# Performance work log

Measured on AMD Instinct MI355X. Metric: run time of the kernel, lower is better.

The kernel has to match this reference:

```python
import jax, jax.numpy as jnp
import numpy as np

EPS = 1e-8
TOP_K = 2


def _l2norm(v, axis=-1):
    # F.normalize: v / max(||v||_2, eps)
    n = jnp.sqrt(jnp.sum(v * v, axis=axis, keepdims=True))
    return v / jnp.maximum(n, EPS)


def setup_inputs() -> dict:
    key = jax.random.key(0)
    ks = jax.random.split(key, 5)
    B, S, D, F, E = 2, 2048, 512, 2048, 8
    x = jax.random.normal(ks[0], (B, S, D), dtype=jnp.float32)
    anchors = jax.random.normal(ks[1], (E, D), dtype=jnp.float32)
    W1 = jax.random.normal(ks[2], (E, D, F), dtype=jnp.float32) * (1.0 / np.sqrt(D))
    b1 = jnp.zeros((E, F), dtype=jnp.float32)
    W2 = jax.random.normal(ks[3], (E, F, D), dtype=jnp.float32) * (1.0 / np.sqrt(F))
    b2 = jnp.zeros((E, D), dtype=jnp.float32)
    return {"x": x, "anchors": anchors, "W1": W1, "b1": b1, "W2": W2, "b2": b2}


def reference(x, anchors, W1, b1, W2, b2):
    B, S, D = x.shape
    E = anchors.shape[0]
    x_flat = x.reshape(B * S, D)  # (T, D)

    # Semantic resonance routing: cosine similarity with anchors
    x_n = _l2norm(x_flat)
    a_n = _l2norm(anchors)
    scores = jnp.einsum('td,ed->te', x_n, a_n)  # (T, E)

    # Noisy top-k (eval mode: no noise) + softmax gates over top-k scores
    topk_scores, topk_idx = jax.lax.top_k(scores, TOP_K)  # (T, K)
    gates = jax.nn.softmax(topk_scores, axis=-1)  # (T, K)

    # Combine weights per (token, expert); top-k indices are distinct per token
    T = B * S
    combine = jnp.zeros((T, E), dtype=x.dtype)
    combine = combine.at[jnp.arange(T)[:, None], topk_idx].add(gates)

    # Per-expert MLP (Linear -> exact GELU -> Linear), combined by gates.
    # Dense-over-experts form is mathematically identical to the sorted
    # grouped dispatch + index_add in the original module.
    h = jnp.einsum('td,edf->tef', x_flat, W1) + b1[None]  # (T, E, F)
    h = jax.nn.gelu(h, approximate=False)
    y = jnp.einsum('tef,efd->ted', h, W2) + b2[None]  # (T, E, D)
    out_flat = jnp.einsum('te,ted->td', combine, y)  # (T, D)

    out = out_flat.reshape(B, S, D)
    # aux_data equivalents: anchors_norm, resonance_scores, topk_indices
    return out, a_n, scores, topk_idx
```

## Files before the change

kernel.cpp:

```cpp
#include <hip/hip_runtime.h>
#include <cstdint>


#define T_TOK 4096
#define D_DIM 512
#define F_DIM 2048
#define E_EXP 8
#define NROWS 9216
#define MAXTILES 72

typedef __bf16 bf16x8 __attribute__((ext_vector_type(8)));
typedef float  f32x4  __attribute__((ext_vector_type(4)));
typedef unsigned short u16;

__device__ __forceinline__ u16 f2b(float f) {
    return __builtin_bit_cast(unsigned short, (__bf16)f);
}
__device__ __forceinline__ void gload16(void* lds, const void* g) {
    __builtin_amdgcn_global_load_lds(
        (const __attribute__((address_space(1))) void*)g,
        (__attribute__((address_space(3))) void*)lds, 16, 0, 0);
}
__device__ __forceinline__ float gelu_f(float v) {
    float z = 0.7978845608f * (v + 0.044715f * v * v * v);
    float t = 1.0f - 2.0f / (1.0f + __expf(2.0f * z));
    return 0.5f * v * (1.0f + t);
}

__global__ void init_k(int* __restrict__ cnt, int* __restrict__ rowmap,
                       float* __restrict__ rowgate, float* __restrict__ outm) {
    int tid = blockIdx.x * 256 + threadIdx.x;
    int nth = gridDim.x * 256;
    if (tid < E_EXP) cnt[tid] = 0;
    for (int i = tid; i < NROWS; i += nth) { rowmap[i] = -1; rowgate[i] = 0.f; }
    float4* o4 = (float4*)outm;
    for (int i = tid; i < (T_TOK * D_DIM) / 4; i += nth)
        o4[i] = float4{0.f, 0.f, 0.f, 0.f};
}

__global__ void anchors_k(const float* __restrict__ anchors,
                          float* __restrict__ an, float* __restrict__ dout_an) {
    int tid = threadIdx.x;
    int lane = tid & 63, e = tid >> 6;
    const float4* ar = (const float4*)(anchors + e * D_DIM + lane * 8);
    float4 v0 = ar[0], v1 = ar[1];
    float ss = v0.x*v0.x + v0.y*v0.y + v0.z*v0.z + v0.w*v0.w
             + v1.x*v1.x + v1.y*v1.y + v1.z*v1.z + v1.w*v1.w;
#pragma unroll
    for (int off = 32; off >= 1; off >>= 1) ss += __shfl_xor(ss, off, 64);
    float inv = 1.0f / fmaxf(sqrtf(ss), 1e-8f);
    float o[8] = {v0.x*inv, v0.y*inv, v0.z*inv, v0.w*inv,
                  v1.x*inv, v1.y*inv, v1.z*inv, v1.w*inv};
#pragma unroll
    for (int i = 0; i < 8; ++i) {
        an[e * D_DIM + lane * 8 + i] = o[i];
        dout_an[e * D_DIM + lane * 8 + i] = o[i];
    }
}

__global__ void routing_k(const float* __restrict__ x, const float* __restrict__ an,
                          float* __restrict__ dout_scores, float* __restrict__ dout_idx,
                          int* __restrict__ idxs, float* __restrict__ gates,
                          int* __restrict__ cnt) {
    __shared__ float anl[E_EXP * 544];
    __shared__ int hist[E_EXP];
    int tid = threadIdx.x;
    if (tid < E_EXP) hist[tid] = 0;
    for (int i = tid; i < E_EXP * D_DIM; i += 256) {
        int e = i >> 9, d = i & 511;
        anl[e * 544 + (d >> 7) * 136 + (d & 127)] = an[i];
    }
    __syncthreads();

    int p = tid & 3;
    int tok = blockIdx.x * 64 + (tid >> 2);
    const float4* xr = (const float4*)(x + (size_t)tok * D_DIM + p * 128);
    const float* ab = &anl[p * 136];
    float dot[E_EXP] = {};
    float ss = 0.f;
    for (int c = 0; c < 32; ++c) {
        float4 xv = xr[c];
        ss += xv.x*xv.x + xv.y*xv.y + xv.z*xv.z + xv.w*xv.w;
#pragma unroll
        for (int e = 0; e < E_EXP; ++e) {
            float4 av = *(const float4*)&ab[e * 544 + c * 4];
            dot[e] += xv.x*av.x + xv.y*av.y + xv.z*av.z + xv.w*av.w;
        }
    }
#pragma unroll
    for (int off = 1; off <= 2; off <<= 1) {
        ss += __shfl_xor(ss, off, 64);
#pragma unroll
        for (int e = 0; e < E_EXP; ++e) dot[e] += __shfl_xor(dot[e], off, 64);
    }

    if (p == 0) {
        float inv = 1.0f / fmaxf(sqrtf(ss), 1e-8f);
        float s[E_EXP];
#pragma unroll
        for (int e = 0; e < E_EXP; ++e) s[e] = dot[e] * inv;
        int i0 = 0; float b0 = s[0];
#pragma unroll
        for (int e = 1; e < E_EXP; ++e) if (s[e] > b0) { b0 = s[e]; i0 = e; }
        int i1 = -1; float b1v = -1e30f;
#pragma unroll
        for (int e = 0; e < E_EXP; ++e)
            if (e != i0 && s[e] > b1v) { b1v = s[e]; i1 = e; }
        if (i1 < 0) { i1 = (i0 + 1) & 7; b1v = s[i1]; }
        float g0 = 1.0f / (1.0f + expf(b1v - b0));
        float g1 = 1.0f - g0;
#pragma unroll
        for (int e = 0; e < E_EXP; ++e) dout_scores[tok * E_EXP + e] = s[e];
        dout_idx[tok * 2 + 0] = (float)i0;
        dout_idx[tok * 2 + 1] = (float)i1;
        idxs[tok * 2 + 0] = i0; idxs[tok * 2 + 1] = i1;
        gates[tok * 2 + 0] = g0; gates[tok * 2 + 1] = g1;
        atomicAdd(&hist[i0], 1);
        atomicAdd(&hist[i1], 1);
    }
    __syncthreads();
    if (tid < E_EXP) atomicAdd(&cnt[tid], hist[tid]);
}

__global__ void offs_k(const int* __restrict__ cnt, int* __restrict__ offs,
                       int* __restrict__ cur) {
    if (threadIdx.x == 0 && blockIdx.x == 0) {
        int acc = 0;
        for (int e = 0; e < E_EXP; ++e) {
            offs[e] = acc; cur[e] = acc;
            acc += (cnt[e] + 127) & ~127;
        }
        offs[E_EXP] = acc;
    }
}

__global__ void assign_k(const int* __restrict__ idxs, const float* __restrict__ gates,
                         int* __restrict__ cur, int* __restrict__ rowmap,
                         float* __restrict__ rowgate) {
    int t = blockIdx.x * 256 + threadIdx.x;
    if (t >= T_TOK) return;
#pragma unroll
    for (int k = 0; k < 2; ++k) {
        int e = idxs[t * 2 + k];
        e = min(max(e, 0), E_EXP - 1);
        int r = atomicAdd(&cur[e], 1);
        if (r >= 0 && r < NROWS) {
            rowmap[r] = t;
            rowgate[r] = gates[t * 2 + k];
        }
    }
}

__global__ void gather_k(const float* __restrict__ x, const int* __restrict__ rowmap,
                         u16* __restrict__ Xg) {
    int r = blockIdx.x;
    int t = rowmap[r];
    int c = threadIdx.x * 2;
    ushort2 o;
    if (t < 0 || t >= T_TOK) { o.x = 0; o.y = 0; }
    else {
        float2 v = *(const float2*)(x + (size_t)t * D_DIM + c);
        o.x = f2b(v.x); o.y = f2b(v.y);
    }
    *(ushort2*)(Xg + (size_t)r * D_DIM + c) = o;
}

__global__ void transpose_cast_k(const float* __restrict__ in, u16* __restrict__ out,
                                 int R, int C) {
    size_t zoff = (size_t)blockIdx.z * R * C;
    in += zoff; out += zoff;
    __shared__ float t[64][65];
    int c0 = blockIdx.x * 64, r0 = blockIdx.y * 64;
    int tid = threadIdx.x;
    int cq = tid & 15, rb = tid >> 4;
#pragma unroll
    for (int pass = 0; pass < 4; ++pass) {
        int rr = rb + pass * 16;
        float4 v = *(const float4*)(in + (size_t)(r0 + rr) * C + c0 + cq * 4);
        t[rr][cq * 4 + 0] = v.x; t[rr][cq * 4 + 1] = v.y;
        t[rr][cq * 4 + 2] = v.z; t[rr][cq * 4 + 3] = v.w;
    }
    __syncthreads();
    int rg = tid & 15, cb = tid >> 4;
#pragma unroll
    for (int pass = 0; pass < 4; ++pass) {
        int c = cb + pass * 16;
        ushort4 o;
        o.x = f2b(t[rg * 4 + 0][c]); o.y = f2b(t[rg * 4 + 1][c]);
        o.z = f2b(t[rg * 4 + 2][c]); o.w = f2b(t[rg * 4 + 3][c]);
        *(ushort4*)(out + (size_t)(c0 + c) * R + r0 + rg * 4) = o;
    }
}

template <int MODE>
__launch_bounds__(256, 4)
__global__ void gemm_k(const u16* __restrict__ A, int lda,
                       const u16* __restrict__ BtBase, int ldb,
                       u16* __restrict__ Hout, const float* __restrict__ b1,
                       float* __restrict__ outm, const float* __restrict__ b2,
                       const int* __restrict__ rowmap, const float* __restrict__ rowgate,
                       const int* __restrict__ offs, int kPer, int nT) {
    int L = blockIdx.x;
    int per = gridDim.x >> 3;
    int tile = (L & 7) * per + (L >> 3);
    int z = 0;
    if (MODE == 1) {
        int half = gridDim.x >> 1;
        z = tile >= half; tile -= z * half;
    }
    int mtile = tile / nT;
    int n0 = (tile - mtile * nT) * 128;
    int row0 = mtile * 128;
    if (row0 >= offs[E_EXP]) return;
    int e = 0;
#pragma unroll
    for (int i = 1; i < E_EXP; ++i) if (row0 >= offs[i]) e = i;
    const u16* Bt = BtBase + (size_t)e * D_DIM * F_DIM;
    int k_begin = z * kPer;
    int k_end = k_begin + kPer;

    alignas(16) __shared__ u16 As[128 * 64];
    alignas(16) __shared__ u16 Bs[128 * 64];

    int tid = threadIdx.x;
    int lane = tid & 63;
    int wv = tid >> 6;
    int wm = wv & 1, wn = wv >> 1;
    int kq = lane >> 4;
    int l15 = lane & 15;

    const u16* aSrc[4]; const u16* bSrc[4];
    u16* aDst[4]; u16* bDst[4];
#pragma unroll
    for (int i = 0; i < 4; ++i) {
        int slot = i * 256 + tid;
        int m = slot >> 3;
        int kc = slot & 7;
        aSrc[i] = A + (size_t)(row0 + m) * lda + kc * 8;
        bSrc[i] = Bt + (size_t)(n0 + m) * ldb + kc * 8;
        aDst[i] = As + slot * 8;
        bDst[i] = Bs + slot * 8;
    }

    f32x4 acc[4][4];
#pragma unroll
    for (int i = 0; i < 4; ++i)
#pragma unroll
        for (int j = 0; j < 4; ++j) acc[i][j] = f32x4{0.f, 0.f, 0.f, 0.f};

    for (int k0 = k_begin; k0 < k_end; k0 += 64) {
#pragma unroll
        for (int i = 0; i < 4; ++i) gload16(aDst[i], aSrc[i] + k0);
#pragma unroll
        for (int i = 0; i < 4; ++i) gload16(bDst[i], bSrc[i] + k0);
        asm volatile("s_waitcnt vmcnt(0)" ::: "memory");
        __syncthreads();
#pragma unroll
        for (int kk = 0; kk < 2; ++kk) {
            int kc = kk * 4 + kq;
            bf16x8 af[4], bfr[4];
#pragma unroll
            for (int i = 0; i < 4; ++i) {
                int rowA = wm * 64 + i * 16 + l15;
                af[i] = *(const bf16x8*)(As + rowA * 64 + kc * 8);
                int rowB = wn * 64 + i * 16 + l15;
                bfr[i] = *(const bf16x8*)(Bs + rowB * 64 + kc * 8);
            }
#pragma unroll
            for (int i = 0; i < 4; ++i)
#pragma unroll
                for (int j = 0; j < 4; ++j)
                    acc[i][j] = __builtin_amdgcn_mfma_f32_16x16x32_bf16(
                        af[i], bfr[j], acc[i][j], 0, 0, 0);
        }
        __syncthreads();
    }

    if constexpr (MODE == 0) {
        const float* b1e = b1 + (size_t)e * F_DIM;
#pragma unroll
        for (int i = 0; i < 4; ++i) {
            int gr = row0 + wm * 64 + i * 16 + kq * 4;
#pragma unroll
            for (int j = 0; j < 4; ++j) {
                int gc = n0 + wn * 64 + j * 16 + l15;
                float bb = b1e[gc];
#pragma unroll
                for (int r = 0; r < 4; ++r) {
                    float v = acc[i][j][r] + bb;
                    Hout[(size_t)(gr + r) * F_DIM + gc] = f2b(gelu_f(v));
                }
            }
        }
    } else {
        const float* b2e = b2 + (size_t)e * D_DIM;
        bool addBias = (k_begin == 0);
#pragma unroll
        for (int i = 0; i < 4; ++i) {
            int grb = row0 + wm * 64 + i * 16 + kq * 4;
#pragma unroll
            for (int r = 0; r < 4; ++r) {
                int tok = rowmap[grb + r];
                float g = rowgate[grb + r];
                if (tok >= 0 && tok < T_TOK) {
                    float* orow = outm + (size_t)tok * D_DIM;
#pragma unroll
                    for (int j = 0; j < 4; ++j) {
                        int gc = n0 + wn * 64 + j * 16 + l15;
                        float bb = addBias ? b2e[gc] : 0.f;
                        atomicAdd(orow + gc, g * (acc[i][j][r] + bb));
                    }
                }
            }
        }
    }
}

#define OFF_AN      0u
#define OFF_CNT     0x10000u
#define OFF_OFFS    0x10100u
#define OFF_CUR     0x10200u
#define OFF_IDX     0x20000u
#define OFF_GATE    0x28000u
#define OFF_ROWMAP  0x30000u
#define OFF_ROWGATE 0x40000u
#define OFF_XG      0x900000u
#define OFF_W1T     0x1200000u
#define OFF_W2T     0x2200000u
#define OFF_HG      0x3200000u

extern "C" void kernel_launch(void* const* d_in, const int* in_sizes, int n_in,
                              void* d_out, int out_size, void* d_ws, size_t ws_size,
                              hipStream_t stream) {
    const float* x       = (const float*)d_in[0];
    const float* anchors = (const float*)d_in[1];
    const float* W1      = (const float*)d_in[2];
    const float* b1      = (const float*)d_in[3];
    const float* W2      = (const float*)d_in[4];
    const float* b2      = (const float*)d_in[5];
    float* out = (float*)d_out;

    char* ws = (char*)d_ws;
    float* an      = (float*)(ws + OFF_AN);
    int*   cnt     = (int*)(ws + OFF_CNT);
    int*   offs    = (int*)(ws + OFF_OFFS);
    int*   cur     = (int*)(ws + OFF_CUR);
    int*   idxs    = (int*)(ws + OFF_IDX);
    float* gates   = (float*)(ws + OFF_GATE);
    int*   rowmap  = (int*)(ws + OFF_ROWMAP);
    float* rowgate = (float*)(ws + OFF_ROWGATE);
    u16*   Xg      = (u16*)(ws + OFF_XG);
    u16*   W1T     = (u16*)(ws + OFF_W1T);
    u16*   W2T     = (u16*)(ws + OFF_W2T);
    u16*   Hg      = (u16*)(ws + OFF_HG);

    float* out_main   = out;
    float* out_an     = out + (size_t)T_TOK * D_DIM;
    float* out_scores = out_an + E_EXP * D_DIM;
    float* out_idx    = out_scores + (size_t)T_TOK * E_EXP;

    init_k<<<512, 256, 0, stream>>>(cnt, rowmap, rowgate, out_main);
    anchors_k<<<1, 512, 0, stream>>>(anchors, an, out_an);
    routing_k<<<T_TOK / 64, 256, 0, stream>>>(x, an, out_scores, out_idx,
                                              idxs, gates, cnt);
    offs_k<<<1, 64, 0, stream>>>(cnt, offs, cur);
    assign_k<<<T_TOK / 256, 256, 0, stream>>>(idxs, gates, cur, rowmap, rowgate);
    gather_k<<<NROWS, 256, 0, stream>>>(x, rowmap, Xg);
    transpose_cast_k<<<dim3(F_DIM / 64, D_DIM / 64, E_EXP), 256, 0, stream>>>(
        W1, W1T, D_DIM, F_DIM);
    transpose_cast_k<<<dim3(D_DIM / 64, F_DIM / 64, E_EXP), 256, 0, stream>>>(
        W2, W2T, F_DIM, D_DIM);
    gemm_k<0><<<16 * MAXTILES, 256, 0, stream>>>(
        Xg, D_DIM, W1T, D_DIM, Hg, b1, nullptr, nullptr,
        rowmap, nullptr, offs, D_DIM, 16);
    gemm_k<1><<<4 * MAXTILES * 2, 256, 0, stream>>>(
        Hg, F_DIM, W2T, F_DIM, nullptr, nullptr, out_main, b2,
        rowmap, rowgate, offs, F_DIM / 2, 4);
}
```

Before: 276.1 us.

## Merge small prep kernels to cut launch count in MoE pipeline

```diff
diff --git a/kernel.cpp b/kernel.cpp
--- a/kernel.cpp
+++ b/kernel.cpp
@@ -28,7 +28,9 @@
 }
 
 __global__ void init_k(int* __restrict__ cnt, int* __restrict__ rowmap,
-                       float* __restrict__ rowgate, float* __restrict__ outm) {
+                       float* __restrict__ rowgate, float* __restrict__ outm,
+                       const float* __restrict__ anchors,
+                       float* __restrict__ an, float* __restrict__ dout_an) {
     int tid = blockIdx.x * 256 + threadIdx.x;
     int nth = gridDim.x * 256;
     if (tid < E_EXP) cnt[tid] = 0;
@@ -36,25 +38,27 @@
     float4* o4 = (float4*)outm;
     for (int i = tid; i < (T_TOK * D_DIM) / 4; i += nth)
         o4[i] = float4{0.f, 0.f, 0.f, 0.f};
-}
-
-__global__ void anchors_k(const float* __restrict__ anchors,
-                          float* __restrict__ an, float* __restrict__ dout_an) {
-    int tid = threadIdx.x;
-    int lane = tid & 63, e = tid >> 6;
-    const float4* ar = (const float4*)(anchors + e * D_DIM + lane * 8);
-    float4 v0 = ar[0], v1 = ar[1];
-    float ss = v0.x*v0.x + v0.y*v0.y + v0.z*v0.z + v0.w*v0.w
-             + v1.x*v1.x + v1.y*v1.y + v1.z*v1.z + v1.w*v1.w;
-#pragma unroll
-    for (int off = 32; off >= 1; off >>= 1) ss += __shfl_xor(ss, off, 64);
-    float inv = 1.0f / fmaxf(sqrtf(ss), 1e-8f);
-    float o[8] = {v0.x*inv, v0.y*inv, v0.z*inv, v0.w*inv,
-                  v1.x*inv, v1.y*inv, v1.z*inv, v1.w*inv};
-#pragma unroll
-    for (int i = 0; i < 8; ++i) {
-        an[e * D_DIM + lane * 8 + i] = o[i];
-        dout_an[e * D_DIM + lane * 8 + i] = o[i];
+    if (blockIdx.x == gridDim.x - 1) {
+        int t = threadIdx.x;
+        int e = t >> 5, l = t & 31;
+        const float4* ar = (const float4*)(anchors + e * D_DIM + l * 16);
+        float4 v0 = ar[0], v1 = ar[1], v2 = ar[2], v3 = ar[3];
+        float ss = v0.x*v0.x + v0.y*v0.y + v0.z*v0.z + v0.w*v0.w
+                 + v1.x*v1.x + v1.y*v1.y + v1.z*v1.z + v1.w*v1.w
+                 + v2.x*v2.x + v2.y*v2.y + v2.z*v2.z + v2.w*v2.w
+                 + v3.x*v3.x + v3.y*v3.y + v3.z*v3.z + v3.w*v3.w;
+#pragma unroll
+        for (int off = 16; off >= 1; off >>= 1) ss += __shfl_xor(ss, off, 32);
+        float inv = 1.0f / fmaxf(sqrtf(ss), 1e-8f);
+        float o[16] = {v0.x*inv, v0.y*inv, v0.z*inv, v0.w*inv,
+                       v1.x*inv, v1.y*inv, v1.z*inv, v1.w*inv,
+                       v2.x*inv, v2.y*inv, v2.z*inv, v2.w*inv,
+                       v3.x*inv, v3.y*inv, v3.z*inv, v3.w*inv};
+#pragma unroll
+        for (int i = 0; i < 16; ++i) {
+            an[e * D_DIM + l * 16 + i] = o[i];
+            dout_an[e * D_DIM + l * 16 + i] = o[i];
+        }
     }
 }
 
@@ -122,56 +126,38 @@
     if (tid < E_EXP) atomicAdd(&cnt[tid], hist[tid]);
 }
 
-__global__ void offs_k(const int* __restrict__ cnt, int* __restrict__ offs,
-                       int* __restrict__ cur) {
-    if (threadIdx.x == 0 && blockIdx.x == 0) {
+__global__ void assign_k(const int* __restrict__ cnt, int* __restrict__ offs,
+                         const int* __restrict__ idxs, const float* __restrict__ gates,
+                         int* __restrict__ rowmap, float* __restrict__ rowgate) {
+    __shared__ int scur[E_EXP];
+    int tid = threadIdx.x;
+    if (tid == 0) {
         int acc = 0;
         for (int e = 0; e < E_EXP; ++e) {
-            offs[e] = acc; cur[e] = acc;
+            offs[e] = acc; scur[e] = acc;
             acc += (cnt[e] + 127) & ~127;
         }
         offs[E_EXP] = acc;
     }
-}
-
-__global__ void assign_k(const int* __restrict__ idxs, const float* __restrict__ gates,
-                         int* __restrict__ cur, int* __restrict__ rowmap,
-                         float* __restrict__ rowgate) {
-    int t = blockIdx.x * 256 + threadIdx.x;
-    if (t >= T_TOK) return;
-#pragma unroll
-    for (int k = 0; k < 2; ++k) {
-        int e = idxs[t * 2 + k];
-        e = min(max(e, 0), E_EXP - 1);
-        int r = atomicAdd(&cur[e], 1);
-        if (r >= 0 && r < NROWS) {
-            rowmap[r] = t;
-            rowgate[r] = gates[t * 2 + k];
-        }
-    }
-}
-
-__global__ void gather_k(const float* __restrict__ x, const int* __restrict__ rowmap,
-                         u16* __restrict__ Xg) {
-    int r = blockIdx.x;
-    int t = rowmap[r];
-    int c = threadIdx.x * 2;
-    ushort2 o;
-    if (t < 0 || t >= T_TOK) { o.x = 0; o.y = 0; }
-    else {
-        float2 v = *(const float2*)(x + (size_t)t * D_DIM + c);
-        o.x = f2b(v.x); o.y = f2b(v.y);
-    }
-    *(ushort2*)(Xg + (size_t)r * D_DIM + c) = o;
-}
-
-__global__ void transpose_cast_k(const float* __restrict__ in, u16* __restrict__ out,
-                                 int R, int C) {
-    size_t zoff = (size_t)blockIdx.z * R * C;
-    in += zoff; out += zoff;
-    __shared__ float t[64][65];
-    int c0 = blockIdx.x * 64, r0 = blockIdx.y * 64;
-    int tid = threadIdx.x;
+    __syncthreads();
+    for (int t = tid; t < T_TOK; t += 1024) {
+#pragma unroll
+        for (int k = 0; k < 2; ++k) {
+            int e = idxs[t * 2 + k];
+            e = min(max(e, 0), E_EXP - 1);
+            int r = atomicAdd(&scur[e], 1);
+            if (r >= 0 && r < NROWS) {
+                rowmap[r] = t;
+                rowgate[r] = gates[t * 2 + k];
+            }
+        }
+    }
+}
+
+__device__ __forceinline__ void tbody(const float* __restrict__ in,
+                                      u16* __restrict__ out, int R, int C,
+                                      int c0, int r0, int tid,
+                                      float (*t)[65]) {
     int cq = tid & 15, rb = tid >> 4;
 #pragma unroll
     for (int pass = 0; pass < 4; ++pass) {
@@ -189,6 +175,40 @@
         o.x = f2b(t[rg * 4 + 0][c]); o.y = f2b(t[rg * 4 + 1][c]);
         o.z = f2b(t[rg * 4 + 2][c]); o.w = f2b(t[rg * 4 + 3][c]);
         *(ushort4*)(out + (size_t)(c0 + c) * R + r0 + rg * 4) = o;
+    }
+}
+
+#define T1_BASE NROWS
+#define T2_BASE (NROWS + 2048)
+#define PREP_BLOCKS (NROWS + 4096)
+
+__global__ void prep_k(const float* __restrict__ x, const int* __restrict__ rowmap,
+                       u16* __restrict__ Xg,
+                       const float* __restrict__ W1, u16* __restrict__ W1T,
+                       const float* __restrict__ W2, u16* __restrict__ W2T) {
+    __shared__ float tsh[64][65];
+    int b = blockIdx.x;
+    int tid = threadIdx.x;
+    if (b < T1_BASE) {
+        int t = rowmap[b];
+        int c = tid * 2;
+        ushort2 o;
+        if (t < 0 || t >= T_TOK) { o.x = 0; o.y = 0; }
+        else {
+            float2 v = *(const float2*)(x + (size_t)t * D_DIM + c);
+            o.x = f2b(v.x); o.y = f2b(v.y);
+        }
+        *(ushort2*)(Xg + (size_t)b * D_DIM + c) = o;
+    } else if (b < T2_BASE) {
+        int tt = b - T1_BASE;
+        int bx = tt & 31, by = (tt >> 5) & 7, bz = tt >> 8;
+        size_t zoff = (size_t)bz * D_DIM * F_DIM;
+        tbody(W1 + zoff, W1T + zoff, D_DIM, F_DIM, bx * 64, by * 64, tid, tsh);
+    } else {
+        int tt = b - T2_BASE;
+        int bx = tt & 7, by = (tt >> 3) & 31, bz = tt >> 8;
+        size_t zoff = (size_t)bz * D_DIM * F_DIM;
+        tbody(W2 + zoff, W2T + zoff, F_DIM, D_DIM, bx * 64, by * 64, tid, tsh);
     }
 }
 
@@ -319,7 +339,6 @@
 #define OFF_AN      0u
 #define OFF_CNT     0x10000u
 #define OFF_OFFS    0x10100u
-#define OFF_CUR     0x10200u
 #define OFF_IDX     0x20000u
 #define OFF_GATE    0x28000u
 #define OFF_ROWMAP  0x30000u
@@ -344,7 +363,6 @@
     float* an      = (float*)(ws + OFF_AN);
     int*   cnt     = (int*)(ws + OFF_CNT);
     int*   offs    = (int*)(ws + OFF_OFFS);
-    int*   cur     = (int*)(ws + OFF_CUR);
     int*   idxs    = (int*)(ws + OFF_IDX);
     float* gates   = (float*)(ws + OFF_GATE);
     int*   rowmap  = (int*)(ws + OFF_ROWMAP);
@@ -359,17 +377,12 @@
     float* out_scores = out_an + E_EXP * D_DIM;
     float* out_idx    = out_scores + (size_t)T_TOK * E_EXP;
 
-    init_k<<<512, 256, 0, stream>>>(cnt, rowmap, rowgate, out_main);
-    anchors_k<<<1, 512, 0, stream>>>(anchors, an, out_an);
+    init_k<<<512, 256, 0, stream>>>(cnt, rowmap, rowgate, out_main,
+                                    anchors, an, out_an);
     routing_k<<<T_TOK / 64, 256, 0, stream>>>(x, an, out_scores, out_idx,
                                               idxs, gates, cnt);
-    offs_k<<<1, 64, 0, stream>>>(cnt, offs, cur);
-    assign_k<<<T_TOK / 256, 256, 0, stream>>>(idxs, gates, cur, rowmap, rowgate);
-    gather_k<<<NROWS, 256, 0, stream>>>(x, rowmap, Xg);
-    transpose_cast_k<<<dim3(F_DIM / 64, D_DIM / 64, E_EXP), 256, 0, stream>>>(
-        W1, W1T, D_DIM, F_DIM);
-    transpose_cast_k<<<dim3(D_DIM / 64, F_DIM / 64, E_EXP), 256, 0, stream>>>(
-        W2, W2T, F_DIM, D_DIM);
+    assign_k<<<1, 1024, 0, stream>>>(cnt, offs, idxs, gates, rowmap, rowgate);
+    prep_k<<<PREP_BLOCKS, 256, 0, stream>>>(x, rowmap, Xg, W1, W1T, W2, W2T);
     gemm_k<0><<<16 * MAXTILES, 256, 0, stream>>>(
         Xg, D_DIM, W1T, D_DIM, Hg, b1, nullptr, nullptr,
         rowmap, nullptr, offs, D_DIM, 16);
```

Result: faster. 243.1 us (-11.9%).
